# Kernel optimization log

Hardware: AMD Instinct MI355X
Metric: run time of the kernel (lower is better)

The kernel has to match this reference:

```python
import jax, jax.numpy as jnp
import numpy as np

T, TRACE, CTX = 4096, 64, 64


def setup_inputs() -> dict:
    key = jax.random.key(0)
    k0, k1, k2, k3 = jax.random.split(key, 4)
    state_re = jax.random.normal(k0, (T, TRACE, CTX), dtype=jnp.float32)
    state_im = jax.random.normal(k1, (T, TRACE, CTX), dtype=jnp.float32)
    x_re = jax.random.normal(k2, (T, TRACE, CTX), dtype=jnp.float32)
    x_im = jax.random.normal(k3, (T, TRACE, CTX), dtype=jnp.float32)
    # deterministic FFA param init (init_deterministic)
    a = jnp.linspace(1e-6, 0.5, TRACE).astype(jnp.float32)
    b = (2.0 * jnp.pi / jnp.linspace(1.0, 1000.0, CTX)).astype(jnp.float32)
    i = jnp.ones((T,), dtype=jnp.int32)          # carry step counter
    j = jnp.arange(T, dtype=jnp.int32)           # incoming time offsets
    return {"state_re": state_re, "state_im": state_im, "x_re": x_re,
            "x_im": x_im, "a": a, "b": b, "i": i, "j": j}


def reference(state_re, state_im, x_re, x_im, a, b, i, j):
    # gamma(t) = exp((-|a| + i*b) * t) expanded in real arithmetic
    t = j.astype(jnp.float32)[:, None, None]              # [T,1,1]
    decay = jnp.exp(-jnp.abs(a)[None, :, None] * t)       # [T,TRACE,1]
    theta = b[None, None, :] * t                          # [T,1,CTX]
    g_re = decay * jnp.cos(theta)                         # [T,TRACE,CTX]
    g_im = decay * jnp.sin(theta)
    # state * gamma + x  (complex multiply-add)
    new_re = state_re * g_re - state_im * g_im + x_re
    new_im = state_re * g_im + state_im * g_re + x_im
    # output: complex state stacked as (..., 2) = (re, im), plus updated counter
    return jnp.stack([new_re, new_im], axis=-1), j + i
```

## Files before the change

kernel.cpp:

```cpp
#include <hip/hip_runtime.h>
#include <math.h>

#define T_DIM 4096
#define TRACE 64
#define CTX   64

__global__ __launch_bounds__(256) void ffm_tables(
    const float* __restrict__ a, const float* __restrict__ b,
    const int*   __restrict__ iv, const int* __restrict__ jv,
    float* __restrict__ tcos, float* __restrict__ tsin,
    float* __restrict__ tdec, float* __restrict__ out_cnt)
{
    const int idx = blockIdx.x * 256 + threadIdx.x;
    const int t   = idx >> 6;
    const int k   = idx & 63;
    const float tf = (float)jv[t];
    float s, c;
    sincosf(b[k] * tf, &s, &c);
    tcos[idx] = c;
    tsin[idx] = s;
    tdec[idx] = expf(-fabsf(a[k]) * tf);
    if (k == 0) out_cnt[t] = (float)(jv[t] + iv[t]);
}

__global__ __launch_bounds__(256, 4) void ffm_main(
    const float* __restrict__ state_re, const float* __restrict__ state_im,
    const float* __restrict__ x_re, const float* __restrict__ x_im,
    const float* __restrict__ tcos, const float* __restrict__ tsin,
    const float* __restrict__ tdec,
    float* __restrict__ out)
{
    const int t   = blockIdx.x;
    const int tid = threadIdx.x;

    const size_t base = (size_t)t * (TRACE * CTX);
    const float4* __restrict__ sre = (const float4*)(state_re + base);
    const float4* __restrict__ sim = (const float4*)(state_im + base);
    const float4* __restrict__ xre = (const float4*)(x_re + base);
    const float4* __restrict__ xim = (const float4*)(x_im + base);
    float4* __restrict__ o = (float4*)(out + base * 2);

    const float4* __restrict__ tc = (const float4*)(tcos + t * 64);
    const float4* __restrict__ ts = (const float4*)(tsin + t * 64);
    const float*  __restrict__ td = tdec + t * 64;

    float4 vre[4], vim[4], vxr[4], vxi[4], vc[4], vs[4];
    float  dec[4];

    #pragma unroll
    for (int k = 0; k < 4; ++k) vre[k] = sre[tid + k * 256];
    #pragma unroll
    for (int k = 0; k < 4; ++k) vim[k] = sim[tid + k * 256];
    #pragma unroll
    for (int k = 0; k < 4; ++k) vxr[k] = xre[tid + k * 256];
    #pragma unroll
    for (int k = 0; k < 4; ++k) vxi[k] = xim[tid + k * 256];
    #pragma unroll
    for (int k = 0; k < 4; ++k) {
        const int g = tid + k * 256;
        vc[k]  = tc[g & 15];
        vs[k]  = ts[g & 15];
        dec[k] = td[g >> 4];
    }
    __builtin_amdgcn_sched_barrier(0);

    #pragma unroll
    for (int k = 0; k < 4; ++k) {
        const int g = tid + k * 256;

        const float gr0 = dec[k] * vc[k].x, gi0 = dec[k] * vs[k].x;
        const float gr1 = dec[k] * vc[k].y, gi1 = dec[k] * vs[k].y;
        const float gr2 = dec[k] * vc[k].z, gi2 = dec[k] * vs[k].z;
        const float gr3 = dec[k] * vc[k].w, gi3 = dec[k] * vs[k].w;

        float4 o0, o1;
        o0.x = fmaf(vre[k].x, gr0, fmaf(-vim[k].x, gi0, vxr[k].x));
        o0.y = fmaf(vre[k].x, gi0, fmaf( vim[k].x, gr0, vxi[k].x));
        o0.z = fmaf(vre[k].y, gr1, fmaf(-vim[k].y, gi1, vxr[k].y));
        o0.w = fmaf(vre[k].y, gi1, fmaf( vim[k].y, gr1, vxi[k].y));
        o1.x = fmaf(vre[k].z, gr2, fmaf(-vim[k].z, gi2, vxr[k].z));
        o1.y = fmaf(vre[k].z, gi2, fmaf( vim[k].z, gr2, vxi[k].z));
        o1.z = fmaf(vre[k].w, gr3, fmaf(-vim[k].w, gi3, vxr[k].w));
        o1.w = fmaf(vre[k].w, gi3, fmaf( vim[k].w, gr3, vxi[k].w));

        o[2 * g + 0] = o0;
        o[2 * g + 1] = o1;
    }
}

__global__ __launch_bounds__(256) void ffm_kernel_fallback(
    const float* __restrict__ state_re, const float* __restrict__ state_im,
    const float* __restrict__ x_re, const float* __restrict__ x_im,
    const float* __restrict__ a, const float* __restrict__ b,
    const int* __restrict__ ivec, const int* __restrict__ jvec,
    float* __restrict__ out, float* __restrict__ out_cnt)
{
    const int t   = blockIdx.x;
    const int tid = threadIdx.x;
    const float tf = (float)jvec[t];

    __shared__ float s_cos[CTX];
    __shared__ float s_sin[CTX];
    __shared__ float s_dec[TRACE];

    if (tid < CTX) {
        float theta = b[tid] * tf;
        float s, c;
        sincosf(theta, &s, &c);
        s_cos[tid] = c;
        s_sin[tid] = s;
    } else if (tid < CTX + TRACE) {
        int tr = tid - CTX;
        s_dec[tr] = expf(-fabsf(a[tr]) * tf);
    }
    if (tid == 0) out_cnt[t] = (float)(jvec[t] + ivec[t]);
    __syncthreads();

    const size_t base = (size_t)t * (TRACE * CTX);
    const float4* sre = (const float4*)(state_re + base);
    const float4* sim = (const float4*)(state_im + base);
    const float4* xre = (const float4*)(x_re + base);
    const float4* xim = (const float4*)(x_im + base);
    float4* o = (float4*)(out + base * 2);

    #pragma unroll
    for (int k = 0; k < 4; ++k) {
        const int g  = tid + k * 256;
        const int e  = g * 4;
        const int tr = e >> 6;
        const int c0 = e & 63;

        const float dec = s_dec[tr];
        const float4 vre = sre[g];
        const float4 vim = sim[g];
        const float4 vxr = xre[g];
        const float4 vxi = xim[g];

        const float gr0 = dec * s_cos[c0 + 0], gi0 = dec * s_sin[c0 + 0];
        const float gr1 = dec * s_cos[c0 + 1], gi1 = dec * s_sin[c0 + 1];
        const float gr2 = dec * s_cos[c0 + 2], gi2 = dec * s_sin[c0 + 2];
        const float gr3 = dec * s_cos[c0 + 3], gi3 = dec * s_sin[c0 + 3];

        float4 o0, o1;
        o0.x = fmaf(vre.x, gr0, fmaf(-vim.x, gi0, vxr.x));
        o0.y = fmaf(vre.x, gi0, fmaf( vim.x, gr0, vxi.x));
        o0.z = fmaf(vre.y, gr1, fmaf(-vim.y, gi1, vxr.y));
        o0.w = fmaf(vre.y, gi1, fmaf( vim.y, gr1, vxi.y));
        o1.x = fmaf(vre.z, gr2, fmaf(-vim.z, gi2, vxr.z));
        o1.y = fmaf(vre.z, gi2, fmaf( vim.z, gr2, vxi.z));
        o1.z = fmaf(vre.w, gr3, fmaf(-vim.w, gi3, vxr.w));
        o1.w = fmaf(vre.w, gi3, fmaf( vim.w, gr3, vxi.w));

        o[2 * g + 0] = o0;
        o[2 * g + 1] = o1;
    }
}

extern "C" void kernel_launch(void* const* d_in, const int* in_sizes, int n_in,
                              void* d_out, int out_size, void* d_ws, size_t ws_size,
                              hipStream_t stream) {
    const float* state_re = (const float*)d_in[0];
    const float* state_im = (const float*)d_in[1];
    const float* x_re     = (const float*)d_in[2];
    const float* x_im     = (const float*)d_in[3];
    const float* a        = (const float*)d_in[4];
    const float* b        = (const float*)d_in[5];
    const int*   iv       = (const int*)d_in[6];
    const int*   jv       = (const int*)d_in[7];

    float* out     = (float*)d_out;
    float* out_cnt = out + (size_t)T_DIM * TRACE * CTX * 2;

    const size_t tab_elems = (size_t)T_DIM * 64;
    const size_t need = 3 * tab_elems * sizeof(float);

    if (ws_size >= need) {
        float* tcos = (float*)d_ws;
        float* tsin = tcos + tab_elems;
        float* tdec = tsin + tab_elems;

        ffm_tables<<<T_DIM * 64 / 256, 256, 0, stream>>>(
            a, b, iv, jv, tcos, tsin, tdec, out_cnt);
        ffm_main<<<T_DIM, 256, 0, stream>>>(
            state_re, state_im, x_re, x_im, tcos, tsin, tdec, out);
    } else {
        ffm_kernel_fallback<<<T_DIM, 256, 0, stream>>>(
            state_re, state_im, x_re, x_im, a, b, iv, jv, out, out_cnt);
    }
}
```

Baseline: 329.4 us.

## Give each wave a contiguous chunk and stagger input-stream load order per wave

Each wave now handles a contiguous 1024-float chunk of the block's slice instead of interleaving across the whole block. This lets the cos/sin table loads be hoisted to a single float4 per thread. The order in which the four input streams are loaded is rotated per wave through a switch, spreading DRAM channel/bank traffic across streams. The launch-bounds occupancy hint and the sched_barrier are removed, which may change register allocation and instruction scheduling, and the switch adds some branch overhead.

```diff
diff --git a/kernel.cpp b/kernel.cpp
--- a/kernel.cpp
+++ b/kernel.cpp
@@ -23,15 +23,18 @@
     if (k == 0) out_cnt[t] = (float)(jv[t] + iv[t]);
 }
 
-__global__ __launch_bounds__(256, 4) void ffm_main(
+__global__ __launch_bounds__(256) void ffm_main(
     const float* __restrict__ state_re, const float* __restrict__ state_im,
     const float* __restrict__ x_re, const float* __restrict__ x_im,
     const float* __restrict__ tcos, const float* __restrict__ tsin,
     const float* __restrict__ tdec,
     float* __restrict__ out)
 {
-    const int t   = blockIdx.x;
-    const int tid = threadIdx.x;
+    const int t    = blockIdx.x;
+    const int tid  = threadIdx.x;
+    const int w    = tid >> 6;
+    const int lane = tid & 63;
+    const int g0   = w * 256 + lane;
 
     const size_t base = (size_t)t * (TRACE * CTX);
     const float4* __restrict__ sre = (const float4*)(state_re + base);
@@ -40,38 +43,34 @@
     const float4* __restrict__ xim = (const float4*)(x_im + base);
     float4* __restrict__ o = (float4*)(out + base * 2);
 
-    const float4* __restrict__ tc = (const float4*)(tcos + t * 64);
-    const float4* __restrict__ ts = (const float4*)(tsin + t * 64);
-    const float*  __restrict__ td = tdec + t * 64;
+    const float4 vc = ((const float4*)(tcos + t * 64))[lane & 15];
+    const float4 vs = ((const float4*)(tsin + t * 64))[lane & 15];
+    const float* td = tdec + t * 64;
+    float dec[4];
+    #pragma unroll
+    for (int k = 0; k < 4; ++k)
+        dec[k] = td[w * 16 + k * 4 + (lane >> 4)];
 
-    float4 vre[4], vim[4], vxr[4], vxi[4], vc[4], vs[4];
-    float  dec[4];
-
-    #pragma unroll
-    for (int k = 0; k < 4; ++k) vre[k] = sre[tid + k * 256];
-    #pragma unroll
-    for (int k = 0; k < 4; ++k) vim[k] = sim[tid + k * 256];
-    #pragma unroll
-    for (int k = 0; k < 4; ++k) vxr[k] = xre[tid + k * 256];
-    #pragma unroll
-    for (int k = 0; k < 4; ++k) vxi[k] = xim[tid + k * 256];
-    #pragma unroll
-    for (int k = 0; k < 4; ++k) {
-        const int g = tid + k * 256;
-        vc[k]  = tc[g & 15];
-        vs[k]  = ts[g & 15];
-        dec[k] = td[g >> 4];
+    float4 vre[4], vim[4], vxr[4], vxi[4];
+#define LD4(dst, src) \
+    dst[0] = src[g0]; dst[1] = src[g0 + 64]; \
+    dst[2] = src[g0 + 128]; dst[3] = src[g0 + 192];
+    switch (w) {
+      case 0: LD4(vre, sre) LD4(vim, sim) LD4(vxr, xre) LD4(vxi, xim) break;
+      case 1: LD4(vim, sim) LD4(vxr, xre) LD4(vxi, xim) LD4(vre, sre) break;
+      case 2: LD4(vxr, xre) LD4(vxi, xim) LD4(vre, sre) LD4(vim, sim) break;
+      default: LD4(vxi, xim) LD4(vre, sre) LD4(vim, sim) LD4(vxr, xre) break;
     }
-    __builtin_amdgcn_sched_barrier(0);
+#undef LD4
 
     #pragma unroll
     for (int k = 0; k < 4; ++k) {
-        const int g = tid + k * 256;
+        const int g = g0 + k * 64;
 
-        const float gr0 = dec[k] * vc[k].x, gi0 = dec[k] * vs[k].x;
-        const float gr1 = dec[k] * vc[k].y, gi1 = dec[k] * vs[k].y;
-        const float gr2 = dec[k] * vc[k].z, gi2 = dec[k] * vs[k].z;
-        const float gr3 = dec[k] * vc[k].w, gi3 = dec[k] * vs[k].w;
+        const float gr0 = dec[k] * vc.x, gi0 = dec[k] * vs.x;
+        const float gr1 = dec[k] * vc.y, gi1 = dec[k] * vs.y;
+        const float gr2 = dec[k] * vc.z, gi2 = dec[k] * vs.z;
+        const float gr3 = dec[k] * vc.w, gi3 = dec[k] * vs.w;
 
         float4 o0, o1;
         o0.x = fmaf(vre[k].x, gr0, fmaf(-vim[k].x, gi0, vxr[k].x));
```

Result: no change. 326.7 us (-0.8%).
